# Optimization experiments

Measured on AMD Instinct MI355X. Metric: run time of the kernel, lower is better.

## Reference

```python
import jax, jax.numpy as jnp
import numpy as np

T, N, E, F0, F1 = 8, 100000, 3200000, 16, 16


def setup_inputs() -> dict:
    key = jax.random.key(0)
    ks = jax.random.split(key, 18)
    inp = {}
    inp["X"] = jax.random.normal(ks[0], (T, N, F0), jnp.float32)
    inp["edge_row"] = jax.random.randint(ks[1], (T, E), 0, N, jnp.int32)
    inp["edge_col"] = jax.random.randint(ks[2], (T, E), 0, N, jnp.int32)
    inp["edge_val"] = jax.random.uniform(ks[3], (T, E), jnp.float32)
    inp["p"] = jax.random.normal(ks[4], (F0,), jnp.float32)
    names = ["W_Z", "U_Z", "B_Z", "W_R", "U_R", "B_R", "W_H", "U_H", "B_H", "W_init"]
    for i, n in enumerate(names):
        inp[n] = jax.random.normal(ks[5 + i], (F0, F1 if n.startswith("B") or n == "W_init" else F0), jnp.float32)
    inp["lin_w"] = jax.random.normal(ks[15], (F1,), jnp.float32)
    inp["lin_b"] = jax.random.normal(ks[16], (1,), jnp.float32)
    return inp


def reference(X, edge_row, edge_col, edge_val, p, W_Z, U_Z, B_Z, W_R, U_R, B_R, W_H, U_H, B_H, W_init, lin_w, lin_b):
    def step(W, xs):
        X_t, row, col, val = xs  # X_t: [N, F0]; row/col/val: [E]
        # summarize: topk-weighted row selection, k = F1
        y = (X_t @ p) / jnp.linalg.norm(p)              # [N]
        yk, idx = jax.lax.top_k(y, F1)                  # sorted desc, matches torch.topk
        Xs = (X_t[idx] * yk[:, None]).T                 # [F0, F1]
        # GRU on the weight matrix W: [F0, F1]
        Zg = jax.nn.sigmoid(W_Z @ Xs + U_Z @ W + B_Z)
        Rg = jax.nn.sigmoid(W_R @ Xs + U_R @ W + B_R)
        Ht = jnp.tanh(W_H @ Xs + U_H @ (Rg * W) + B_H)
        W_new = (1.0 - Zg) * W + Zg * Ht
        # sparse GCONV: (A @ X_t) @ W_new via gather + segment_sum
        AH = jax.ops.segment_sum(val[:, None] * X_t[col], row, num_segments=N)  # [N, F0]
        H_new = AH @ W_new                              # [N, F1]
        return W_new, H_new

    _, Y = jax.lax.scan(step, W_init, (X, edge_row, edge_col, edge_val))  # Y: [T, N, F1]
    return Y @ lin_w + lin_b[0]                          # [T, N]
```

## Files before the change

### kernel.cpp

```cpp
#include <hip/hip_runtime.h>
#include <stdint.h>

#define T_STEPS 8
#define N_NODES 100000
#define E_EDGES 3200000
#define NB1 250
#define CHUNK 400
#define NB3 391
#define NCAND_T 4000
#define NSLICE 8
#define ESLICE (E_EDGES / NSLICE)
#define NRNG 4
#define ACCN 25000
#define SC_BLKS (T_STEPS * NRNG * NSLICE)

__device__ __forceinline__ uint16_t f2bf(float x) {
    uint32_t b = __float_as_uint(x);
    b += 0x7FFFu + ((b >> 16) & 1u);
    return (uint16_t)(b >> 16);
}
__device__ __forceinline__ float bf2f(uint16_t u) {
    return __uint_as_float(((uint32_t)u) << 16);
}

__device__ __forceinline__ unsigned long long make_key(float v, int idx) {
    uint32_t u = __float_as_uint(v);
    u = (u & 0x80000000u) ? ~u : (u | 0x80000000u);
    return (((unsigned long long)u) << 32) | (unsigned long long)(~(uint32_t)idx);
}
__device__ __forceinline__ float key_val(unsigned long long k) {
    uint32_t u = (uint32_t)(k >> 32);
    u = (u & 0x80000000u) ? (u & 0x7FFFFFFFu) : ~u;
    return __uint_as_float(u);
}
__device__ __forceinline__ int key_idx(unsigned long long k) {
    return (int)(~(uint32_t)(k & 0xFFFFFFFFu));
}

__device__ __forceinline__ unsigned long long shfl_xor_u64(unsigned long long x, int mask) {
    uint32_t lo = (uint32_t)x, hi = (uint32_t)(x >> 32);
    lo = __shfl_xor((unsigned int)lo, mask);
    hi = __shfl_xor((unsigned int)hi, mask);
    return (((unsigned long long)hi) << 32) | lo;
}

__device__ __forceinline__ void wave_argmax(unsigned long long& m, int& mp) {
    #pragma unroll
    for (int off = 32; off; off >>= 1) {
        unsigned long long o = shfl_xor_u64(m, off);
        int op = __shfl_xor(mp, off);
        if (o > m) { m = o; mp = op; }
    }
}

__device__ __forceinline__ float dot16(const float4* __restrict__ xr, const float* w) {
    float4 a = xr[0], b = xr[1], c = xr[2], d = xr[3];
    return a.x*w[0] + a.y*w[1] + a.z*w[2] + a.w*w[3]
         + b.x*w[4] + b.y*w[5] + b.z*w[6] + b.w*w[7]
         + c.x*w[8] + c.y*w[9] + c.z*w[10] + c.w*w[11]
         + d.x*w[12] + d.y*w[13] + d.z*w[14] + d.w*w[15];
}

__global__ __launch_bounds__(256) void k_y_topk_all(const float* __restrict__ X,
                                                    const float* __restrict__ p,
                                                    unsigned long long* __restrict__ cand) {
    __shared__ unsigned long long keys[CHUNK];
    __shared__ unsigned long long wm[4];
    __shared__ int wp[4];
    int tid = threadIdx.x;
    int t = blockIdx.x / NB1;
    int b = blockIdx.x % NB1;
    const float* Xt = X + (size_t)t * N_NODES * 16;
    float pv[16];
    #pragma unroll
    for (int i = 0; i < 16; i++) pv[i] = p[i];
    float pn = 0.f;
    #pragma unroll
    for (int i = 0; i < 16; i++) pn += pv[i] * pv[i];
    float inv = 1.0f / sqrtf(pn);
    int base = b * CHUNK;
    for (int i = tid; i < CHUNK; i += 256) {
        int n = base + i;
        float y = dot16((const float4*)(Xt + (size_t)n * 16), pv) * inv;
        keys[i] = make_key(y, n);
    }
    __syncthreads();
    for (int k = 0; k < 16; k++) {
        unsigned long long m = 0ULL; int mp = -1;
        for (int i = tid; i < CHUNK; i += 256) {
            unsigned long long v = keys[i];
            if (v > m) { m = v; mp = i; }
        }
        wave_argmax(m, mp);
        if ((tid & 63) == 0) { wm[tid >> 6] = m; wp[tid >> 6] = mp; }
        __syncthreads();
        if (tid == 0) {
            unsigned long long best = wm[0]; int bp = wp[0];
            #pragma unroll
            for (int w2 = 1; w2 < 4; w2++) if (wm[w2] > best) { best = wm[w2]; bp = wp[w2]; }
            cand[(size_t)t * NCAND_T + b * 16 + k] = best;
            keys[bp] = 0ULL;
        }
        __syncthreads();
    }
}

__global__ __launch_bounds__(512) void k_merge_gru(
    const unsigned long long* __restrict__ cand,
    const float* __restrict__ X,
    const float* __restrict__ Winit,
    const float* __restrict__ W_Z, const float* __restrict__ U_Z, const float* __restrict__ B_Z,
    const float* __restrict__ W_R, const float* __restrict__ U_R, const float* __restrict__ B_R,
    const float* __restrict__ W_H, const float* __restrict__ U_H, const float* __restrict__ B_H,
    const float* __restrict__ lin_w,
    float* __restrict__ weff_g) {
    __shared__ float mWZ[256], mUZ[256], mBZ[256], mWR[256], mUR[256], mBR[256];
    __shared__ float mWH[256], mUH[256], mBH[256], mLW[16];
    __shared__ int   sidx[8][16];
    __shared__ float sval[8][16];
    __shared__ float Xs_all[8][16][16];
    __shared__ float Wcur[16][16];
    __shared__ float RgW[16][16];
    int tid = threadIdx.x;
    if (tid < 256) {
        mWZ[tid] = W_Z[tid]; mUZ[tid] = U_Z[tid]; mBZ[tid] = B_Z[tid];
        mWR[tid] = W_R[tid]; mUR[tid] = U_R[tid]; mBR[tid] = B_R[tid];
        mWH[tid] = W_H[tid]; mUH[tid] = U_H[tid]; mBH[tid] = B_H[tid];
        Wcur[tid >> 4][tid & 15] = Winit[tid];
        if (tid < 16) mLW[tid] = lin_w[tid];
    }
    {
        int w = tid >> 6, lane = tid & 63;
        const unsigned long long* ct = cand + (size_t)w * NCAND_T;
        int cb = lane * 4;
        unsigned long long h0 = 0, h1 = 0, h2 = 0, h3 = 0;
        int p0 = 0, p1 = 0, p2 = 0, p3 = 0;
        if (cb + 0 < NB1) h0 = ct[(cb + 0) * 16];
        if (cb + 1 < NB1) h1 = ct[(cb + 1) * 16];
        if (cb + 2 < NB1) h2 = ct[(cb + 2) * 16];
        if (cb + 3 < NB1) h3 = ct[(cb + 3) * 16];
        for (int k = 0; k < 16; k++) {
            unsigned long long m = h0; int pay = (lane << 2) | 0;
            if (h1 > m) { m = h1; pay = (lane << 2) | 1; }
            if (h2 > m) { m = h2; pay = (lane << 2) | 2; }
            if (h3 > m) { m = h3; pay = (lane << 2) | 3; }
            wave_argmax(m, pay);
            if (lane == 0) { sidx[w][k] = key_idx(m); sval[w][k] = key_val(m); }
            if ((pay >> 2) == lane) {
                switch (pay & 3) {
                case 0: p0++; h0 = (p0 < 16) ? ct[(cb + 0) * 16 + p0] : 0ULL; break;
                case 1: p1++; h1 = (p1 < 16) ? ct[(cb + 1) * 16 + p1] : 0ULL; break;
                case 2: p2++; h2 = (p2 < 16) ? ct[(cb + 2) * 16 + p2] : 0ULL; break;
                default: p3++; h3 = (p3 < 16) ? ct[(cb + 3) * 16 + p3] : 0ULL; break;
                }
            }
        }
    }
    __syncthreads();
    for (int e = tid; e < 8 * 256; e += 512) {
        int tt = e >> 8, kk = (e >> 4) & 15, ff = e & 15;
        Xs_all[tt][ff][kk] = X[(size_t)tt * N_NODES * 16 + (size_t)sidx[tt][kk] * 16 + ff]
                           * sval[tt][kk];
    }
    __syncthreads();
    int i = (tid & 255) >> 4, j = tid & 15;
    for (int t = 0; t < T_STEPS; t++) {
        float Zg = 0.f, wn = 0.f;
        if (tid < 256) {
            float az = 0.f, ar = 0.f, uz = 0.f, ur = 0.f;
            #pragma unroll
            for (int m = 0; m < 16; m++) {
                az += mWZ[i * 16 + m] * Xs_all[t][m][j];
                ar += mWR[i * 16 + m] * Xs_all[t][m][j];
                uz += mUZ[i * 16 + m] * Wcur[m][j];
                ur += mUR[i * 16 + m] * Wcur[m][j];
            }
            Zg = 1.0f / (1.0f + expf(-(az + uz + mBZ[i * 16 + j])));
            float Rg = 1.0f / (1.0f + expf(-(ar + ur + mBR[i * 16 + j])));
            RgW[i][j] = Rg * Wcur[i][j];
        }
        __syncthreads();
        if (tid < 256) {
            float ah = 0.f, uh = 0.f;
            #pragma unroll
            for (int m = 0; m < 16; m++) {
                ah += mWH[i * 16 + m] * Xs_all[t][m][j];
                uh += mUH[i * 16 + m] * RgW[m][j];
            }
            float Ht = tanhf(ah + uh + mBH[i * 16 + j]);
            wn = (1.0f - Zg) * Wcur[i][j] + Zg * Ht;
        }
        __syncthreads();
        if (tid < 256) Wcur[i][j] = wn;
        __syncthreads();
        if (tid < 16) {
            float acc = 0.f;
            #pragma unroll
            for (int jj = 0; jj < 16; jj++) acc += Wcur[tid][jj] * mLW[jj];
            weff_g[t * 16 + tid] = acc;
        }
        __syncthreads();
    }
}

__global__ __launch_bounds__(256) void k_s_all(const float* __restrict__ X,
                                               const float* __restrict__ weff,
                                               float* __restrict__ s) {
    int t = blockIdx.x / NB3;
    int b = blockIdx.x % NB3;
    __shared__ float w[16];
    if (threadIdx.x < 16) w[threadIdx.x] = weff[t * 16 + threadIdx.x];
    __syncthreads();
    int n = b * 256 + threadIdx.x;
    if (n < N_NODES) {
        float v = dot16((const float4*)(X + ((size_t)t * N_NODES + n) * 16), w);
        s[(size_t)t * N_NODES + n] = v;
    }
}

#define PROCESS(Rr, Cc, Vv, OK) do {                                           \
    bool m0 = (OK) && ((Rr.x & 3) == r);                                       \
    bool m1 = (OK) && ((Rr.y & 3) == r);                                       \
    bool m2 = (OK) && ((Rr.z & 3) == r);                                       \
    bool m3 = (OK) && ((Rr.w & 3) == r);                                       \
    int  l0 = Rr.x >> 2, l1 = Rr.y >> 2, l2 = Rr.z >> 2, l3 = Rr.w >> 2;       \
    float g0 = m0 ? st[Cc.x] : 0.f;                                            \
    float g1 = m1 ? st[Cc.y] : 0.f;                                            \
    float g2 = m2 ? st[Cc.z] : 0.f;                                            \
    float g3 = m3 ? st[Cc.w] : 0.f;                                            \
    if (m0) atomicAdd(&acc[l0], Vv.x * g0);                                    \
    if (m1) atomicAdd(&acc[l1], Vv.y * g1);                                    \
    if (m2) atomicAdd(&acc[l2], Vv.z * g2);                                    \
    if (m3) atomicAdd(&acc[l3], Vv.w * g3);                                    \
} while (0)

extern "C" __global__ __launch_bounds__(1024) void k_scatter_fused(
    const int* __restrict__ erow, const int* __restrict__ ecol,
    const float* __restrict__ evalv, const float* __restrict__ s,
    uint16_t* __restrict__ rep) {
    extern __shared__ float acc[];
    const int bid = blockIdx.x;
    const int t = bid & 7;
    const int m = bid >> 3;
    const int slice = m >> 2;
    const int r = m & 3;
    const int tid = threadIdx.x;
    for (int i = tid; i < ACCN; i += 1024) acc[i] = 0.f;
    __syncthreads();
    const float* __restrict__ st = s + (size_t)t * N_NODES;
    const size_t eb = (size_t)t * E_EDGES + (size_t)slice * ESLICE;
    const int4* __restrict__ r4 = (const int4*)(erow + eb);
    const int4* __restrict__ c4 = (const int4*)(ecol + eb);
    const float4* __restrict__ v4 = (const float4*)(evalv + eb);
    const int n4 = ESLICE / 4;
    const int S = (n4 + 1023) >> 10;

    int j0 = tid;
    int jc0 = j0 < n4 ? j0 : n4 - 1;
    int4 R0 = r4[jc0]; int4 C0 = c4[jc0]; float4 V0 = v4[jc0];

    #pragma unroll 1
    for (int k = 0; k < S; k += 2) {
        int j1 = tid + ((k + 1) << 10);
        int jc1 = j1 < n4 ? j1 : n4 - 1;
        int4 R1 = r4[jc1]; int4 C1 = c4[jc1]; float4 V1 = v4[jc1];
        __builtin_amdgcn_sched_barrier(0);
        bool ok0 = (tid + (k << 10)) < n4;
        PROCESS(R0, C0, V0, ok0);
        __builtin_amdgcn_sched_barrier(0);
        int j2 = tid + ((k + 2) << 10);
        int jc2 = j2 < n4 ? j2 : n4 - 1;
        R0 = r4[jc2]; C0 = c4[jc2]; V0 = v4[jc2];
        __builtin_amdgcn_sched_barrier(0);
        bool ok1 = (tid + ((k + 1) << 10)) < n4;
        PROCESS(R1, C1, V1, ok1);
        __builtin_amdgcn_sched_barrier(0);
    }
    __syncthreads();
    const int seg = t * 32 + m;
    uint16_t* rp = rep + (size_t)seg * ACCN;
    for (int i = tid; i < ACCN; i += 1024) rp[i] = f2bf(acc[i]);
}

__global__ __launch_bounds__(256) void k_reduce_full(const uint16_t* __restrict__ rep,
                                                     const float* __restrict__ lin_b,
                                                     float* __restrict__ out) {
    int t = blockIdx.x / NB3;
    int b = blockIdx.x % NB3;
    int n = b * 256 + threadIdx.x;
    if (n >= N_NODES) return;
    int r = n & 3;
    int local = n >> 2;
    float acc = lin_b[0];
    #pragma unroll
    for (int sl = 0; sl < NSLICE; sl++) {
        int seg = t * 32 + sl * 4 + r;
        acc += bf2f(rep[(size_t)seg * ACCN + local]);
    }
    out[(size_t)t * N_NODES + n] = acc;
}

extern "C" void kernel_launch(void* const* d_in, const int* in_sizes, int n_in,
                              void* d_out, int out_size, void* d_ws, size_t ws_size,
                              hipStream_t stream) {
    const float* X     = (const float*)d_in[0];
    const int*   erow  = (const int*)d_in[1];
    const int*   ecol  = (const int*)d_in[2];
    const float* evalv = (const float*)d_in[3];
    const float* p     = (const float*)d_in[4];
    const float* W_Z   = (const float*)d_in[5];
    const float* U_Z   = (const float*)d_in[6];
    const float* B_Z   = (const float*)d_in[7];
    const float* W_R   = (const float*)d_in[8];
    const float* U_R   = (const float*)d_in[9];
    const float* B_R   = (const float*)d_in[10];
    const float* W_H   = (const float*)d_in[11];
    const float* U_H   = (const float*)d_in[12];
    const float* B_H   = (const float*)d_in[13];
    const float* Winit = (const float*)d_in[14];
    const float* lin_w = (const float*)d_in[15];
    const float* lin_b = (const float*)d_in[16];
    float* out = (float*)d_out;

    size_t dynLDS = (size_t)ACCN * sizeof(float);
    (void)hipFuncSetAttribute((const void*)k_scatter_fused,
                              hipFuncAttributeMaxDynamicSharedMemorySize,
                              (int)dynLDS);

    char* ws = (char*)d_ws;
    float* s    = (float*)ws;
    float* weff = (float*)(ws + 3200000);
    unsigned long long* cand = (unsigned long long*)(ws + 3201024);
    uint16_t* rep = (uint16_t*)(ws + 3457024);

    k_y_topk_all<<<T_STEPS * NB1, 256, 0, stream>>>(X, p, cand);
    k_merge_gru<<<1, 512, 0, stream>>>(cand, X, Winit,
                                       W_Z, U_Z, B_Z, W_R, U_R, B_R, W_H, U_H, B_H,
                                       lin_w, weff);
    k_s_all<<<T_STEPS * NB3, 256, 0, stream>>>(X, weff, s);
    k_scatter_fused<<<SC_BLKS, 1024, dynLDS, stream>>>(erow, ecol, evalv, s, rep);
    k_reduce_full<<<T_STEPS * NB3, 256, 0, stream>>>(rep, lin_b, out);
}
```

Baseline: 279.9 us.

## Split scatter row space into 8 ranges and simplify edge loop

Doubles the number of row-range partitions in the fused scatter kernel, halving each block's LDS accumulator to 12500 floats. This should let more blocks share a CU, but every block now streams the whole edge slice while keeping only one eighth of it, so edge-read traffic doubles. The manually software-pipelined loop with sched barriers and prefetch is replaced by a plain strided loop. The reduce kernel is updated to the new segment layout, and the dynamic LDS attribute call is dropped because 50KB no longer needs it.

```diff
diff --git a/kernel.cpp b/kernel.cpp
--- a/kernel.cpp
+++ b/kernel.cpp
@@ -10,9 +10,9 @@
 #define NCAND_T 4000
 #define NSLICE 8
 #define ESLICE (E_EDGES / NSLICE)
-#define NRNG 4
-#define ACCN 25000
-#define SC_BLKS (T_STEPS * NRNG * NSLICE)
+#define NRNG 8
+#define ACCN 12500
+#define SC_BLKS (T_STEPS * NSLICE * NRNG)
 
 __device__ __forceinline__ uint16_t f2bf(float x) {
     uint32_t b = __float_as_uint(x);
@@ -218,22 +218,6 @@
     }
 }
 
-#define PROCESS(Rr, Cc, Vv, OK) do {                                           \
-    bool m0 = (OK) && ((Rr.x & 3) == r);                                       \
-    bool m1 = (OK) && ((Rr.y & 3) == r);                                       \
-    bool m2 = (OK) && ((Rr.z & 3) == r);                                       \
-    bool m3 = (OK) && ((Rr.w & 3) == r);                                       \
-    int  l0 = Rr.x >> 2, l1 = Rr.y >> 2, l2 = Rr.z >> 2, l3 = Rr.w >> 2;       \
-    float g0 = m0 ? st[Cc.x] : 0.f;                                            \
-    float g1 = m1 ? st[Cc.y] : 0.f;                                            \
-    float g2 = m2 ? st[Cc.z] : 0.f;                                            \
-    float g3 = m3 ? st[Cc.w] : 0.f;                                            \
-    if (m0) atomicAdd(&acc[l0], Vv.x * g0);                                    \
-    if (m1) atomicAdd(&acc[l1], Vv.y * g1);                                    \
-    if (m2) atomicAdd(&acc[l2], Vv.z * g2);                                    \
-    if (m3) atomicAdd(&acc[l3], Vv.w * g3);                                    \
-} while (0)
-
 extern "C" __global__ __launch_bounds__(1024) void k_scatter_fused(
     const int* __restrict__ erow, const int* __restrict__ ecol,
     const float* __restrict__ evalv, const float* __restrict__ s,
@@ -242,8 +226,8 @@
     const int bid = blockIdx.x;
     const int t = bid & 7;
     const int m = bid >> 3;
-    const int slice = m >> 2;
-    const int r = m & 3;
+    const int slice = m >> 3;
+    const int r = m & 7;
     const int tid = threadIdx.x;
     for (int i = tid; i < ACCN; i += 1024) acc[i] = 0.f;
     __syncthreads();
@@ -253,31 +237,18 @@
     const int4* __restrict__ c4 = (const int4*)(ecol + eb);
     const float4* __restrict__ v4 = (const float4*)(evalv + eb);
     const int n4 = ESLICE / 4;
-    const int S = (n4 + 1023) >> 10;
-
-    int j0 = tid;
-    int jc0 = j0 < n4 ? j0 : n4 - 1;
-    int4 R0 = r4[jc0]; int4 C0 = c4[jc0]; float4 V0 = v4[jc0];
-
-    #pragma unroll 1
-    for (int k = 0; k < S; k += 2) {
-        int j1 = tid + ((k + 1) << 10);
-        int jc1 = j1 < n4 ? j1 : n4 - 1;
-        int4 R1 = r4[jc1]; int4 C1 = c4[jc1]; float4 V1 = v4[jc1];
-        __builtin_amdgcn_sched_barrier(0);
-        bool ok0 = (tid + (k << 10)) < n4;
-        PROCESS(R0, C0, V0, ok0);
-        __builtin_amdgcn_sched_barrier(0);
-        int j2 = tid + ((k + 2) << 10);
-        int jc2 = j2 < n4 ? j2 : n4 - 1;
-        R0 = r4[jc2]; C0 = c4[jc2]; V0 = v4[jc2];
-        __builtin_amdgcn_sched_barrier(0);
-        bool ok1 = (tid + ((k + 1) << 10)) < n4;
-        PROCESS(R1, C1, V1, ok1);
-        __builtin_amdgcn_sched_barrier(0);
-    }
-    __syncthreads();
-    const int seg = t * 32 + m;
+
+    for (int i = tid; i < n4; i += 1024) {
+        int4 R = r4[i];
+        int4 C = c4[i];
+        float4 V = v4[i];
+        if ((R.x & 7) == r) atomicAdd(&acc[R.x >> 3], V.x * st[C.x]);
+        if ((R.y & 7) == r) atomicAdd(&acc[R.y >> 3], V.y * st[C.y]);
+        if ((R.z & 7) == r) atomicAdd(&acc[R.z >> 3], V.z * st[C.z]);
+        if ((R.w & 7) == r) atomicAdd(&acc[R.w >> 3], V.w * st[C.w]);
+    }
+    __syncthreads();
+    const int seg = t * 64 + m;
     uint16_t* rp = rep + (size_t)seg * ACCN;
     for (int i = tid; i < ACCN; i += 1024) rp[i] = f2bf(acc[i]);
 }
@@ -289,12 +260,12 @@
     int b = blockIdx.x % NB3;
     int n = b * 256 + threadIdx.x;
     if (n >= N_NODES) return;
-    int r = n & 3;
-    int local = n >> 2;
+    int r = n & 7;
+    int local = n >> 3;
     float acc = lin_b[0];
     #pragma unroll
     for (int sl = 0; sl < NSLICE; sl++) {
-        int seg = t * 32 + sl * 4 + r;
+        int seg = t * 64 + sl * 8 + r;
         acc += bf2f(rep[(size_t)seg * ACCN + local]);
     }
     out[(size_t)t * N_NODES + n] = acc;
@@ -323,9 +294,6 @@
     float* out = (float*)d_out;
 
     size_t dynLDS = (size_t)ACCN * sizeof(float);
-    (void)hipFuncSetAttribute((const void*)k_scatter_fused,
-                              hipFuncAttributeMaxDynamicSharedMemorySize,
-                              (int)dynLDS);
 
     char* ws = (char*)d_ws;
     float* s    = (float*)ws;
```

Measured after the change: 350.1 us. 1.25x slower.
